# Optimization experiments

Hardware: AMD Instinct MI355X
Metric: run time of the kernel (lower is better)

## Reference

```python
import jax, jax.numpy as jnp
import numpy as np

N = 8192
D = 512            # d_model
E = 8              # num_experts
H = 1024           # expert_hidden_dim
RH = 256           # router_hidden_dim
TOPK = 2
IN_DIM = 9 * D + 3
LN_EPS = 1e-5


def layernorm(x, g, b, eps=LN_EPS):
    m = jnp.mean(x, axis=-1, keepdims=True)
    v = jnp.mean((x - m) ** 2, axis=-1, keepdims=True)
    return (x - m) * jax.lax.rsqrt(v + eps) * g + b


def setup_inputs() -> dict:
    key = jax.random.key(0)
    ks = jax.random.split(key, 16)
    s_in = 1.0 / np.sqrt(IN_DIM)
    s_rh = 1.0 / np.sqrt(RH)
    s_h = 1.0 / np.sqrt(H)
    return {
        "z1": jax.random.normal(ks[0], (N, D), jnp.float32),
        "z2": jax.random.normal(ks[1], (N, D), jnp.float32),
        "z3": jax.random.normal(ks[2], (N, D), jnp.float32),
        "mask": jnp.ones((N, 3), jnp.float32),
        # LayerNorms
        "ln_g": jnp.ones((D,), jnp.float32), "ln_b": jnp.zeros((D,), jnp.float32),
        "lnp_g": jnp.ones((D,), jnp.float32), "lnp_b": jnp.zeros((D,), jnp.float32),
        "oln_g": jnp.ones((D,), jnp.float32), "oln_b": jnp.zeros((D,), jnp.float32),
        # Router MLP
        "r_w1": jax.random.normal(ks[3], (IN_DIM, RH), jnp.float32) * s_in,
        "r_b1": jnp.zeros((RH,), jnp.float32),
        "r_w2": jax.random.normal(ks[4], (RH, E), jnp.float32) * s_rh,
        "r_b2": jnp.zeros((E,), jnp.float32),
        "log_temp": jnp.array(np.log(1.0), jnp.float32),
        # Stacked experts: fc1 [E, IN_DIM, H], fc2 [E, H, D]
        "e_w1": jax.random.normal(ks[5], (E, IN_DIM, H), jnp.float32) * s_in,
        "e_b1": jnp.zeros((E, H), jnp.float32),
        "e_w2": jax.random.normal(ks[6], (E, H, D), jnp.float32) * s_h,
        "e_b2": jnp.zeros((E, D), jnp.float32),
    }


def reference(z1, z2, z3, mask, ln_g, ln_b, lnp_g, lnp_b, oln_g, oln_b,
              r_w1, r_b1, r_w2, r_b2, log_temp, e_w1, e_b1, e_w2, e_b2):
    # --- build fusion input ---
    z1n = layernorm(z1, ln_g, ln_b)
    z2n = layernorm(z2, ln_g, ln_b)
    z3n = layernorm(z3, ln_g, ln_b)
    d12 = layernorm(z1n - z2n, lnp_g, lnp_b)
    d13 = layernorm(z1n - z3n, lnp_g, lnp_b)
    d23 = layernorm(z2n - z3n, lnp_g, lnp_b)
    p12 = layernorm(z1n * z2n, lnp_g, lnp_b)
    p13 = layernorm(z1n * z3n, lnp_g, lnp_b)
    p23 = layernorm(z2n * z3n, lnp_g, lnp_b)
    x = jnp.concatenate([z1n, z2n, z3n, d12, d13, d23, p12, p13, p23, mask], axis=-1)  # [N, 9D+3]

    # --- router: MLP + temperature-scaled top-k softmax ---
    temp = jnp.clip(jnp.exp(log_temp), 1e-3, 100.0)
    rh = jax.nn.gelu(x @ r_w1 + r_b1, approximate=False)
    logits = (rh @ r_w2 + r_b2) / temp                      # [N, E]
    topv, topi = jax.lax.top_k(logits, TOPK)
    keep = jnp.zeros_like(logits).at[jnp.arange(logits.shape[0])[:, None], topi].set(1.0)
    masked_logits = jnp.where(keep == 0, -jnp.inf, logits)
    gate = jax.nn.softmax(masked_logits, axis=-1)           # [N, E]

    # --- dense expert compute (matches torch.stack over experts) ---
    eh = jax.nn.gelu(jnp.einsum('ni,eih->neh', x, e_w1) + e_b1, approximate=False)
    outs = jnp.einsum('neh,ehd->ned', eh, e_w2) + e_b2      # [N, E, D]
    z = jnp.einsum('ne,ned->nd', gate, outs)                # combine

    # --- masked residual ---
    denom = jnp.clip(jnp.sum(mask, axis=1, keepdims=True), 1.0, None)
    z_res = (mask[:, 0:1] * z1n + mask[:, 1:2] * z2n + mask[:, 2:3] * z3n) / denom
    z = z + z_res

    return layernorm(z, oln_g, oln_b)
```

## Files before the change

kernel.cpp:

```cpp
#include <hip/hip_runtime.h>
#include <math.h>

#define N_TOK 8192
#define DMODEL 512
#define NEXP 8
#define HEXP 1024
#define RHDIM 256
#define KP 4672
#define IN_REAL 4611
#define BK 64
#define NPAIR (N_TOK * 2)
#define MAXT 136

typedef unsigned short u16;
typedef __bf16 bf16x8 __attribute__((ext_vector_type(8)));
typedef float f32x4 __attribute__((ext_vector_type(4)));

__device__ inline u16 f2bf(float f) {
    union { float f; unsigned u; } x; x.f = f;
    unsigned r = x.u + 0x7FFFu + ((x.u >> 16) & 1u);
    return (u16)(r >> 16);
}
__device__ inline float bf2f(u16 u) {
    union { unsigned u; float f; } x; x.u = ((unsigned)u) << 16;
    return x.f;
}
__device__ inline float gelu_exact(float v) {
    return 0.5f * v * (1.f + erff(v * 0.70710678118654752440f));
}

__device__ inline void async_cp16(const u16* g, u16* l) {
    __builtin_amdgcn_global_load_lds(
        (const __attribute__((address_space(1))) unsigned int*)g,
        (__attribute__((address_space(3))) unsigned int*)l, 16, 0, 0);
}

template<int M>
__device__ inline void breduce(float (&v)[M], int tid, float* red) {
    #pragma unroll
    for (int o = 32; o > 0; o >>= 1)
        #pragma unroll
        for (int i = 0; i < M; i++) v[i] += __shfl_xor(v[i], o);
    __syncthreads();
    if ((tid & 63) == 0) {
        #pragma unroll
        for (int i = 0; i < M; i++) red[(tid >> 6) * M + i] = v[i];
    }
    __syncthreads();
    if (tid < M) {
        float S = 0.f;
        #pragma unroll
        for (int w8 = 0; w8 < 8; w8++) S += red[w8 * M + tid];
        red[96 + tid] = S;
    }
    __syncthreads();
    #pragma unroll
    for (int i = 0; i < M; i++) v[i] = red[96 + i];
}

__device__ inline float2 bstats512(float v, int tid, float* red) {
    float s = v, q = v * v;
    #pragma unroll
    for (int o = 32; o > 0; o >>= 1) {
        s += __shfl_xor(s, o);
        q += __shfl_xor(q, o);
    }
    __syncthreads();
    if ((tid & 63) == 0) { red[(tid >> 6) * 2] = s; red[(tid >> 6) * 2 + 1] = q; }
    __syncthreads();
    if (tid == 0) {
        float S = 0.f, Q = 0.f;
        #pragma unroll
        for (int i = 0; i < 8; i++) { S += red[i * 2]; Q += red[i * 2 + 1]; }
        float m = S * (1.f / 512.f);
        float var = fmaxf(Q * (1.f / 512.f) - m * m, 0.f);
        red[16] = m;
        red[17] = rsqrtf(var + 1e-5f);
    }
    __syncthreads();
    return make_float2(red[16], red[17]);
}

__global__ __launch_bounds__(256)
void transpose_f32_bf16(const float* __restrict__ src, u16* __restrict__ dhi, u16* __restrict__ dlo,
                        int K0, int KPd, int H, size_t sbatch, size_t dbatch) {
    __shared__ float tile[32][33];
    int bz = blockIdx.z;
    src += (size_t)bz * sbatch;
    size_t dob = (size_t)bz * dbatch;
    int k0 = blockIdx.x * 32, h0 = blockIdx.y * 32;
    int tx = threadIdx.x, ty = threadIdx.y;
    for (int i = ty; i < 32; i += 8) {
        int k = k0 + i;
        tile[i][tx] = (k < K0) ? src[(size_t)k * H + (h0 + tx)] : 0.f;
    }
    __syncthreads();
    for (int i = ty; i < 32; i += 8) {
        int h = h0 + i, k = k0 + tx;
        float v = tile[tx][i];
        u16 hv = f2bf(v);
        dhi[dob + (size_t)h * KPd + k] = hv;
        if (dlo) dlo[dob + (size_t)h * KPd + k] = f2bf(v - bf2f(hv));
    }
}

__global__ __launch_bounds__(512)
void build_x(const float* __restrict__ z1, const float* __restrict__ z2, const float* __restrict__ z3,
             const float* __restrict__ mask,
             const float* __restrict__ ln_g, const float* __restrict__ ln_b,
             const float* __restrict__ lnp_g, const float* __restrict__ lnp_b,
             u16* __restrict__ xhi, u16* __restrict__ xlo) {
    __shared__ float red[108];
    int n = blockIdx.x, d = threadIdx.x;
    float a = z1[(size_t)n * DMODEL + d];
    float b = z2[(size_t)n * DMODEL + d];
    float c = z3[(size_t)n * DMODEL + d];
    float gg = ln_g[d], bb = ln_b[d], pg = lnp_g[d], pb = lnp_b[d];
    size_t base = (size_t)n * KP;

    auto emit = [&](int seg, float v) {
        u16 h = f2bf(v);
        xhi[base + seg * DMODEL + d] = h;
        xlo[base + seg * DMODEL + d] = f2bf(v - bf2f(h));
    };
    auto lnv = [](float v, float s, float q, float g, float bo) {
        float m = s * (1.f / 512.f);
        float var = fmaxf(q * (1.f / 512.f) - m * m, 0.f);
        return (v - m) * rsqrtf(var + 1e-5f) * g + bo;
    };
    float v6[6] = {a, a * a, b, b * b, c, c * c};
    breduce<6>(v6, d, red);
    float z1n = lnv(a, v6[0], v6[1], gg, bb);
    float z2n = lnv(b, v6[2], v6[3], gg, bb);
    float z3n = lnv(c, v6[4], v6[5], gg, bb);
    emit(0, z1n); emit(1, z2n); emit(2, z3n);
    float d12 = z1n - z2n, d13 = z1n - z3n, d23 = z2n - z3n;
    float p12 = z1n * z2n, p13 = z1n * z3n, p23 = z2n * z3n;
    float v12[12] = {d12, d12 * d12, d13, d13 * d13, d23, d23 * d23,
                     p12, p12 * p12, p13, p13 * p13, p23, p23 * p23};
    breduce<12>(v12, d, red);
    emit(3, lnv(d12, v12[0], v12[1], pg, pb));
    emit(4, lnv(d13, v12[2], v12[3], pg, pb));
    emit(5, lnv(d23, v12[4], v12[5], pg, pb));
    emit(6, lnv(p12, v12[6], v12[7], pg, pb));
    emit(7, lnv(p13, v12[8], v12[9], pg, pb));
    emit(8, lnv(p23, v12[10], v12[11], pg, pb));
    if (d < 64) {
        int col = 9 * DMODEL + d;
        float v = (d < 3) ? mask[(size_t)n * 3 + d] : 0.f;
        u16 h = f2bf(v);
        xhi[base + col] = h;
        xlo[base + col] = f2bf(v - bf2f(h));
    }
}


#define GEMM_DEFS                                                             \
    int t = threadIdx.x;                                                      \
    int lane = t & 63, w = t >> 6;                                            \
    int r8 = lane >> 3;                                                       \
    int ce = ((lane & 7) ^ r8) * 8;         \
    int fr = lane & 15, q4 = lane >> 4;                                       \
    int wm = (w & 1) * 64, wn = (w >> 1) * 64;                                \
    f32x4 acc[4][4];                                                          \
    { f32x4 z4 = {0.f, 0.f, 0.f, 0.f};                                        \
      _Pragma("unroll") for (int i = 0; i < 4; i++)                           \
      _Pragma("unroll") for (int j = 0; j < 4; j++) acc[i][j] = z4; }         \
    u16 *lAp[2], *lBp[4];                                                     \
    _Pragma("unroll") for (int i = 0; i < 2; i++)                             \
        lAp[i] = lA + (w * 16 + 8 * i) * BK;                                  \
    _Pragma("unroll") for (int i = 0; i < 4; i++)                             \
        lBp[i] = lB + (w * 32 + 8 * i) * BK;

#define GEMM_KSTEP                                                            \
        __syncthreads();                                                      \
        _Pragma("unroll") for (int i = 0; i < 2; i++) {                       \
            async_cp16(gA[i], lAp[i]); gA[i] += BK;                           \
        }                                                                     \
        _Pragma("unroll") for (int i = 0; i < 4; i++) {                       \
            async_cp16(gB[i], lBp[i]); gB[i] += BK;                           \
        }                                                                     \
        __syncthreads();                                                      \
        _Pragma("unroll") for (int ks = 0; ks < 2; ks++) {                    \
            bf16x8 af[4], bfr[4];                                             \
            int cofs = (((q4 + ks * 4) ^ (fr & 7)) * 8);                      \
            _Pragma("unroll") for (int i = 0; i < 4; i++)                     \
                af[i] = *(const bf16x8*)&lA[(wm + i * 16 + fr) * BK + cofs];  \
            _Pragma("unroll") for (int j = 0; j < 4; j++)                     \
                bfr[j] = *(const bf16x8*)&lB[(wn + j * 16 + fr) * BK + cofs]; \
            _Pragma("unroll") for (int i = 0; i < 4; i++)                     \
            _Pragma("unroll") for (int j = 0; j < 4; j++)                     \
                acc[i][j] = __builtin_amdgcn_mfma_f32_16x16x32_bf16(af[i], bfr[j], acc[i][j], 0, 0, 0); \
        }

__global__ __launch_bounds__(512, 4)
void router_fc1(const u16* __restrict__ xhi, const u16* __restrict__ xlo,
                const u16* __restrict__ rw1hi, const u16* __restrict__ rw1lo,
                float* __restrict__ rpart) {
    int mt = blockIdx.x & 63, part = blockIdx.x >> 6;
    int region = part >> 1, half = part & 1;
    const u16* A = (region == 2) ? xlo : xhi;
    const u16* B = (region == 1) ? rw1lo : rw1hi;
    int kbase = half ? 2304 : 0;
    int klen  = half ? 2368 : 2304;

    __shared__ u16 lA[128 * BK];
    __shared__ u16 lB[256 * BK];
    GEMM_DEFS

    const u16* gA[2]; const u16* gB[4];
    #pragma unroll
    for (int i = 0; i < 2; i++)
        gA[i] = A + (size_t)(mt * 128 + w * 16 + 8 * i + r8) * KP + kbase + ce;
    #pragma unroll
    for (int i = 0; i < 4; i++)
        gB[i] = B + (size_t)(w * 32 + 8 * i + r8) * KP + kbase + ce;

    for (int k0 = 0; k0 < klen; k0 += BK) {
        GEMM_KSTEP
    }
    float* outp = rpart + (size_t)part * ((size_t)N_TOK * RHDIM);
    int cn = lane & 15;
    #pragma unroll
    for (int i = 0; i < 4; i++)
        #pragma unroll
        for (int rr = 0; rr < 4; rr++) {
            int mg = mt * 128 + wm + i * 16 + q4 * 4 + rr;
            #pragma unroll
            for (int j = 0; j < 4; j++)
                outp[(size_t)mg * RHDIM + wn + j * 16 + cn] = acc[i][j][rr];
        }
}

__global__ __launch_bounds__(256)
void logits_topk(const float* __restrict__ rpart, const float* __restrict__ r_b1,
                 const float* __restrict__ r_w2, const float* __restrict__ r_b2,
                 const float* __restrict__ log_temp,
                 float* __restrict__ pgate, int* __restrict__ pexp,
                 int* __restrict__ lists, int* __restrict__ counts) {
    int t = threadIdx.x, wave = t >> 6, lane = t & 63;
    int n = blockIdx.x * 4 + wave;
    float4 v = {0.f, 0.f, 0.f, 0.f};
    #pragma unroll
    for (int p = 0; p < 6; p++) {
        float4 s = ((const float4*)(rpart + (size_t)p * ((size_t)N_TOK * RHDIM) + (size_t)n * RHDIM))[lane];
        v.x += s.x; v.y += s.y; v.z += s.z; v.w += s.w;
    }
    float4 b1 = ((const float4*)r_b1)[lane];
    float rh0 = gelu_exact(v.x + b1.x);
    float rh1 = gelu_exact(v.y + b1.y);
    float rh2 = gelu_exact(v.z + b1.z);
    float rh3 = gelu_exact(v.w + b1.w);
    int k = lane * 4;
    float p8[8];
    #pragma unroll
    for (int e = 0; e < 8; e++)
        p8[e] = rh0 * r_w2[(k + 0) * 8 + e] + rh1 * r_w2[(k + 1) * 8 + e]
              + rh2 * r_w2[(k + 2) * 8 + e] + rh3 * r_w2[(k + 3) * 8 + e];
    #pragma unroll
    for (int o = 32; o > 0; o >>= 1)
        #pragma unroll
        for (int e = 0; e < 8; e++) p8[e] += __shfl_xor(p8[e], o);
    if (lane == 0) {
        float temp = fminf(fmaxf(expf(log_temp[0]), 1e-3f), 100.f);
        float l[8];
        #pragma unroll
        for (int e = 0; e < 8; e++) l[e] = (p8[e] + r_b2[e]) / temp;
        int i1 = 0;
        #pragma unroll
        for (int i = 1; i < 8; i++) if (l[i] > l[i1]) i1 = i;
        int i2 = (i1 == 0) ? 1 : 0;
        #pragma unroll
        for (int i = 0; i < 8; i++) if (i != i1 && l[i] > l[i2]) i2 = i;
        float p = expf(l[i2] - l[i1]);
        float g1 = 1.f / (1.f + p);
        float g2 = p / (1.f + p);
        pgate[n * 2] = g1;     pexp[n * 2] = i1;
        pgate[n * 2 + 1] = g2; pexp[n * 2 + 1] = i2;
        int pos1 = atomicAdd(&counts[i1], 1);
        lists[(size_t)i1 * N_TOK + pos1] = n * 2;
        int pos2 = atomicAdd(&counts[i2], 1);
        lists[(size_t)i2 * N_TOK + pos2] = n * 2 + 1;
    }
}

__global__ void sched_tiles(const int* __restrict__ counts, int* __restrict__ tiles) {
    if (threadIdx.x == 0) {
        int tcount = 0;
        for (int e = 0; e < NEXP; e++) {
            int nt = (counts[e] + 127) >> 7;
            for (int mt = 0; mt < nt; mt++) tiles[tcount++] = (e << 16) | mt;
        }
        for (; tcount < MAXT; tcount++) tiles[tcount] = -1;
    }
}

__global__ __launch_bounds__(512, 4)
void expert_fc1(const u16* __restrict__ xhi, const u16* __restrict__ w1t,
                const float* __restrict__ e_b1, const int* __restrict__ lists,
                const int* __restrict__ counts, const int* __restrict__ tiles,
                u16* __restrict__ eh) {
    int nt = blockIdx.x & 3, ti = blockIdx.x >> 2;
    int info = tiles[ti];
    if (info < 0) return;
    int e = info >> 16, mt = info & 0xFFFF;
    int cnt = counts[e];

    __shared__ u16 lA[128 * BK];
    __shared__ u16 lB[256 * BK];
    __shared__ int rows[128];
    int tt = threadIdx.x;
    if (tt < 128) {
        int m = mt * 128 + tt;
        rows[tt] = lists[(size_t)e * N_TOK + (m < cnt ? m : 0)];
    }
    __syncthreads();

    GEMM_DEFS

    const u16* wb = w1t + (size_t)e * HEXP * KP + (size_t)(nt * 256) * KP;
    const u16* gA[2]; const u16* gB[4];
    #pragma unroll
    for (int i = 0; i < 2; i++)
        gA[i] = xhi + (size_t)(rows[w * 16 + 8 * i + r8] >> 1) * KP + ce;
    #pragma unroll
    for (int i = 0; i < 4; i++)
        gB[i] = wb + (size_t)(w * 32 + 8 * i + r8) * KP + ce;

    for (int k0 = 0; k0 < KP; k0 += BK) {
        GEMM_KSTEP
    }
    int cn = lane & 15;
    #pragma unroll
    for (int i = 0; i < 4; i++)
        #pragma unroll
        for (int rr = 0; rr < 4; rr++) {
            int ml = wm + i * 16 + q4 * 4 + rr;
            int mg = mt * 128 + ml;
            if (mg < cnt) {
                int entry = rows[ml];
                #pragma unroll
                for (int j = 0; j < 4; j++) {
                    int col = nt * 256 + wn + j * 16 + cn;
                    float v = acc[i][j][rr] + e_b1[(size_t)e * HEXP + col];
                    eh[(size_t)entry * HEXP + col] = f2bf(gelu_exact(v));
                }
            }
        }
}

__global__ __launch_bounds__(512, 4)
void expert_fc2(const u16* __restrict__ eh, const u16* __restrict__ w2t,
                const int* __restrict__ lists, const int* __restrict__ counts,
                const int* __restrict__ tiles, float* __restrict__ outs) {
    int nt = blockIdx.x & 1, ti = blockIdx.x >> 1;
    int info = tiles[ti];
    if (info < 0) return;
    int e = info >> 16, mt = info & 0xFFFF;
    int cnt = counts[e];

    __shared__ u16 lA[128 * BK];
    __shared__ u16 lB[256 * BK];
    __shared__ int rows[128];
    int tt = threadIdx.x;
    if (tt < 128) {
        int m = mt * 128 + tt;
        rows[tt] = lists[(size_t)e * N_TOK + (m < cnt ? m : 0)];
    }
    __syncthreads();

    GEMM_DEFS

    const u16* wb = w2t + (size_t)e * DMODEL * HEXP + (size_t)(nt * 256) * HEXP;
    const u16* gA[2]; const u16* gB[4];
    #pragma unroll
    for (int i = 0; i < 2; i++)
        gA[i] = eh + (size_t)rows[w * 16 + 8 * i + r8] * HEXP + ce;
    #pragma unroll
    for (int i = 0; i < 4; i++)
        gB[i] = wb + (size_t)(w * 32 + 8 * i + r8) * HEXP + ce;

    for (int k0 = 0; k0 < HEXP; k0 += BK) {
        GEMM_KSTEP
    }
    int cn = lane & 15;
    #pragma unroll
    for (int i = 0; i < 4; i++)
        #pragma unroll
        for (int rr = 0; rr < 4; rr++) {
            int ml = wm + i * 16 + q4 * 4 + rr;
            int mg = mt * 128 + ml;
            if (mg < cnt) {
                int entry = rows[ml];
                #pragma unroll
                for (int j = 0; j < 4; j++) {
                    int col = nt * 256 + wn + j * 16 + cn;
                    outs[(size_t)entry * DMODEL + col] = acc[i][j][rr];
                }
            }
        }
}

__global__ __launch_bounds__(512)
void combine_ln(const float* __restrict__ outs, const float* __restrict__ pgate,
                const int* __restrict__ pexp, const float* __restrict__ e_b2,
                const float* __restrict__ mask, const u16* __restrict__ xhi,
                const u16* __restrict__ xlo, const float* __restrict__ oln_g,
                const float* __restrict__ oln_b, float* __restrict__ out) {
    __shared__ float red[18];
    int n = blockIdx.x, d = threadIdx.x;
    float g0 = pgate[n * 2], g1 = pgate[n * 2 + 1];
    int e0 = pexp[n * 2], e1 = pexp[n * 2 + 1];
    float o = g0 * (outs[(size_t)(n * 2) * DMODEL + d] + e_b2[(size_t)e0 * DMODEL + d])
            + g1 * (outs[(size_t)(n * 2 + 1) * DMODEL + d] + e_b2[(size_t)e1 * DMODEL + d]);
    float m0 = mask[n * 3 + 0], m1 = mask[n * 3 + 1], m2 = mask[n * 3 + 2];
    float denom = fmaxf(m0 + m1 + m2, 1.f);
    size_t xb = (size_t)n * KP;
    float z1n = bf2f(xhi[xb + d]) + bf2f(xlo[xb + d]);
    float z2n = bf2f(xhi[xb + DMODEL + d]) + bf2f(xlo[xb + DMODEL + d]);
    float z3n = bf2f(xhi[xb + 2 * DMODEL + d]) + bf2f(xlo[xb + 2 * DMODEL + d]);
    float z = o + (m0 * z1n + m1 * z2n + m2 * z3n) / denom;
    float2 st = bstats512(z, d, red);
    out[(size_t)n * DMODEL + d] = (z - st.x) * st.y * oln_g[d] + oln_b[d];
}

extern "C" void kernel_launch(void* const* d_in, const int* in_sizes, int n_in,
                              void* d_out, int out_size, void* d_ws, size_t ws_size,
                              hipStream_t stream) {
    (void)in_sizes; (void)n_in; (void)out_size; (void)ws_size;
    const float* z1       = (const float*)d_in[0];
    const float* z2       = (const float*)d_in[1];
    const float* z3       = (const float*)d_in[2];
    const float* mask     = (const float*)d_in[3];
    const float* ln_g     = (const float*)d_in[4];
    const float* ln_b     = (const float*)d_in[5];
    const float* lnp_g    = (const float*)d_in[6];
    const float* lnp_b    = (const float*)d_in[7];
    const float* oln_g    = (const float*)d_in[8];
    const float* oln_b    = (const float*)d_in[9];
    const float* r_w1     = (const float*)d_in[10];
    const float* r_b1     = (const float*)d_in[11];
    const float* r_w2     = (const float*)d_in[12];
    const float* r_b2     = (const float*)d_in[13];
    const float* log_temp = (const float*)d_in[14];
    const float* e_w1     = (const float*)d_in[15];
    const float* e_b1     = (const float*)d_in[16];
    const float* e_w2     = (const float*)d_in[17];
    const float* e_b2     = (const float*)d_in[18];
    float* out = (float*)d_out;

    char* p = (char*)d_ws;
    auto carve = [&](size_t bytes) { char* r = p; p += (bytes + 255) & ~(size_t)255; return r; };
    u16*   xhi    = (u16*)carve((size_t)N_TOK * KP * 2);
    u16*   xlo    = (u16*)carve((size_t)N_TOK * KP * 2);
    u16*   w1t    = (u16*)carve((size_t)NEXP * HEXP * KP * 2);
    u16*   w2t    = (u16*)carve((size_t)NEXP * DMODEL * HEXP * 2);
    u16*   rw1hi  = (u16*)carve((size_t)RHDIM * KP * 2);
    u16*   rw1lo  = (u16*)carve((size_t)RHDIM * KP * 2);
    float* rpart  = (float*)carve((size_t)6 * N_TOK * RHDIM * 4);
    u16*   eh     = (u16*)carve((size_t)NPAIR * HEXP * 2);
    float* outsb  = (float*)carve((size_t)NPAIR * DMODEL * 4);
    float* pgate  = (float*)carve((size_t)NPAIR * 4);
    int*   pexp   = (int*)carve((size_t)NPAIR * 4);
    int*   lists  = (int*)carve((size_t)NEXP * N_TOK * 4);
    int*   counts = (int*)carve(256);
    int*   tiles  = (int*)carve(MAXT * 4);

    dim3 tb(32, 8);
    transpose_f32_bf16<<<dim3(KP / 32, HEXP / 32, NEXP), tb, 0, stream>>>(
        e_w1, w1t, (u16*)nullptr, IN_REAL, KP, HEXP, (size_t)IN_REAL * HEXP, (size_t)HEXP * KP);
    transpose_f32_bf16<<<dim3(HEXP / 32, DMODEL / 32, NEXP), tb, 0, stream>>>(
        e_w2, w2t, (u16*)nullptr, HEXP, HEXP, DMODEL, (size_t)HEXP * DMODEL, (size_t)DMODEL * HEXP);
    transpose_f32_bf16<<<dim3(KP / 32, RHDIM / 32, 1), tb, 0, stream>>>(
        r_w1, rw1hi, rw1lo, IN_REAL, KP, RHDIM, (size_t)0, (size_t)0);

    build_x<<<N_TOK, 512, 0, stream>>>(z1, z2, z3, mask, ln_g, ln_b, lnp_g, lnp_b, xhi, xlo);

    router_fc1<<<384, 512, 0, stream>>>(xhi, xlo, rw1hi, rw1lo, rpart);

    hipMemsetAsync(counts, 0, 256, stream);
    logits_topk<<<N_TOK / 4, 256, 0, stream>>>(rpart, r_b1, r_w2, r_b2, log_temp,
                                               pgate, pexp, lists, counts);
    sched_tiles<<<1, 64, 0, stream>>>(counts, tiles);

    expert_fc1<<<MAXT * 4, 512, 0, stream>>>(xhi, w1t, e_b1, lists, counts, tiles, eh);
    expert_fc2<<<MAXT * 2, 512, 0, stream>>>(eh, w2t, lists, counts, tiles, outsb);

    combine_ln<<<N_TOK, 512, 0, stream>>>(outsb, pgate, pexp, e_b2, mask, xhi, xlo, oln_g, oln_b, out);
}
```

Measured before the change: 991.5 us.

## Triple-buffer LDS tiles with async prefetch in router and expert GEMMs

Replaces the single-buffered load-sync-compute loop in the router fc1 and both expert GEMMs with a 3-stage LDS ring. Async global-to-LDS copies are issued three K-steps ahead, and vmcnt waits let loads overlap the MFMA work. Fragments are read into registers before the next stage is issued, and the MFMA block runs at raised wave priority. LDS use triples (about 144KB per block), so launch bounds drop from 4 to 2 blocks per CU. This trades occupancy for latency hiding, and the clamped tail prefetch repeats redundant loads.

```diff
diff --git a/kernel.cpp b/kernel.cpp
--- a/kernel.cpp
+++ b/kernel.cpp
@@ -155,9 +155,12 @@
 }
 
 
-#define GEMM_DEFS                                                             \
-    int t = threadIdx.x;                                                      \
-    int lane = t & 63, w = t >> 6;                                            \
+#define ASZ (128 * BK)
+#define BSZ (256 * BK)
+
+#define PIPE_DEFS                                                             \
+    int t_ = threadIdx.x;                                                     \
+    int lane = t_ & 63, w = t_ >> 6;                                          \
     int r8 = lane >> 3;                                                       \
     int ce = ((lane & 7) ^ r8) * 8;         \
     int fr = lane & 15, q4 = lane >> 4;                                       \
@@ -166,34 +169,54 @@
     { f32x4 z4 = {0.f, 0.f, 0.f, 0.f};                                        \
       _Pragma("unroll") for (int i = 0; i < 4; i++)                           \
       _Pragma("unroll") for (int j = 0; j < 4; j++) acc[i][j] = z4; }         \
-    u16 *lAp[2], *lBp[4];                                                     \
+    u16 *lApA[2], *lApB[4];                                                   \
     _Pragma("unroll") for (int i = 0; i < 2; i++)                             \
-        lAp[i] = lA + (w * 16 + 8 * i) * BK;                                  \
+        lApA[i] = lA + (w * 16 + 8 * i) * BK;                                 \
     _Pragma("unroll") for (int i = 0; i < 4; i++)                             \
-        lBp[i] = lB + (w * 32 + 8 * i) * BK;
-
-#define GEMM_KSTEP                                                            \
-        __syncthreads();                                                      \
-        _Pragma("unroll") for (int i = 0; i < 2; i++) {                       \
-            async_cp16(gA[i], lAp[i]); gA[i] += BK;                           \
-        }                                                                     \
-        _Pragma("unroll") for (int i = 0; i < 4; i++) {                       \
-            async_cp16(gB[i], lBp[i]); gB[i] += BK;                           \
-        }                                                                     \
-        __syncthreads();                                                      \
+        lApB[i] = lB + (w * 32 + 8 * i) * BK;
+
+#define PIPE_STAGE(buf_, kk_)                                                 \
+    { int ko_ = (kk_) * BK;                                                   \
+      _Pragma("unroll") for (int i = 0; i < 2; i++)                           \
+          async_cp16(gA[i] + ko_, lApA[i] + (buf_) * ASZ);                    \
+      _Pragma("unroll") for (int i = 0; i < 4; i++)                           \
+          async_cp16(gB[i] + ko_, lApB[i] + (buf_) * BSZ); }
+
+#define PIPE_LOOP(NT_)                                                        \
+    PIPE_STAGE(0, 0)                                                          \
+    PIPE_STAGE(1, 1)                                                          \
+    PIPE_STAGE(2, 2)                                                          \
+    int cur = 0;                                                              \
+    for (int kt = 0; kt < (NT_); kt++) {                                      \
+        asm volatile("s_waitcnt vmcnt(12)" ::: "memory");                     \
+        __builtin_amdgcn_sched_barrier(0);                                    \
+        __builtin_amdgcn_s_barrier();                                         \
+        const u16* cA = lA + cur * ASZ;                                       \
+        const u16* cB = lB + cur * BSZ;                                       \
+        bf16x8 af[2][4], bfr[2][4];                                           \
         _Pragma("unroll") for (int ks = 0; ks < 2; ks++) {                    \
-            bf16x8 af[4], bfr[4];                                             \
             int cofs = (((q4 + ks * 4) ^ (fr & 7)) * 8);                      \
             _Pragma("unroll") for (int i = 0; i < 4; i++)                     \
-                af[i] = *(const bf16x8*)&lA[(wm + i * 16 + fr) * BK + cofs];  \
+                af[ks][i] = *(const bf16x8*)&cA[(wm + i * 16 + fr) * BK + cofs]; \
             _Pragma("unroll") for (int j = 0; j < 4; j++)                     \
-                bfr[j] = *(const bf16x8*)&lB[(wn + j * 16 + fr) * BK + cofs]; \
-            _Pragma("unroll") for (int i = 0; i < 4; i++)                     \
-            _Pragma("unroll") for (int j = 0; j < 4; j++)                     \
-                acc[i][j] = __builtin_amdgcn_mfma_f32_16x16x32_bf16(af[i], bfr[j], acc[i][j], 0, 0, 0); \
-        }
-
-__global__ __launch_bounds__(512, 4)
+                bfr[ks][j] = *(const bf16x8*)&cB[(wn + j * 16 + fr) * BK + cofs]; \
+        }                                                                     \
+        asm volatile("s_waitcnt lgkmcnt(0)" ::: "memory");                    \
+        __builtin_amdgcn_sched_barrier(0);                                    \
+        __builtin_amdgcn_s_barrier();                                         \
+        int nk = kt + 3; if (nk >= (NT_)) nk = (NT_) - 1;                     \
+        PIPE_STAGE(cur, nk)                                                   \
+        __builtin_amdgcn_sched_barrier(0);                                    \
+        __builtin_amdgcn_s_setprio(1);                                        \
+        _Pragma("unroll") for (int ks = 0; ks < 2; ks++)                      \
+        _Pragma("unroll") for (int i = 0; i < 4; i++)                         \
+        _Pragma("unroll") for (int j = 0; j < 4; j++)                         \
+            acc[i][j] = __builtin_amdgcn_mfma_f32_16x16x32_bf16(af[ks][i], bfr[ks][j], acc[i][j], 0, 0, 0); \
+        __builtin_amdgcn_s_setprio(0);                                        \
+        cur = (cur == 2) ? 0 : cur + 1;                                       \
+    }
+
+__global__ __launch_bounds__(512, 2)
 void router_fc1(const u16* __restrict__ xhi, const u16* __restrict__ xlo,
                 const u16* __restrict__ rw1hi, const u16* __restrict__ rw1lo,
                 float* __restrict__ rpart) {
@@ -204,9 +227,9 @@
     int kbase = half ? 2304 : 0;
     int klen  = half ? 2368 : 2304;
 
-    __shared__ u16 lA[128 * BK];
-    __shared__ u16 lB[256 * BK];
-    GEMM_DEFS
+    __shared__ u16 lA[3 * ASZ];
+    __shared__ u16 lB[3 * BSZ];
+    PIPE_DEFS
 
     const u16* gA[2]; const u16* gB[4];
     #pragma unroll
@@ -216,9 +239,9 @@
     for (int i = 0; i < 4; i++)
         gB[i] = B + (size_t)(w * 32 + 8 * i + r8) * KP + kbase + ce;
 
-    for (int k0 = 0; k0 < klen; k0 += BK) {
-        GEMM_KSTEP
-    }
+    int nt = klen / BK;
+    PIPE_LOOP(nt)
+
     float* outp = rpart + (size_t)part * ((size_t)N_TOK * RHDIM);
     int cn = lane & 15;
     #pragma unroll
@@ -295,7 +318,7 @@
     }
 }
 
-__global__ __launch_bounds__(512, 4)
+__global__ __launch_bounds__(512, 2)
 void expert_fc1(const u16* __restrict__ xhi, const u16* __restrict__ w1t,
                 const float* __restrict__ e_b1, const int* __restrict__ lists,
                 const int* __restrict__ counts, const int* __restrict__ tiles,
@@ -306,8 +329,8 @@
     int e = info >> 16, mt = info & 0xFFFF;
     int cnt = counts[e];
 
-    __shared__ u16 lA[128 * BK];
-    __shared__ u16 lB[256 * BK];
+    __shared__ u16 lA[3 * ASZ];
+    __shared__ u16 lB[3 * BSZ];
     __shared__ int rows[128];
     int tt = threadIdx.x;
     if (tt < 128) {
@@ -316,7 +339,7 @@
     }
     __syncthreads();
 
-    GEMM_DEFS
+    PIPE_DEFS
 
     const u16* wb = w1t + (size_t)e * HEXP * KP + (size_t)(nt * 256) * KP;
     const u16* gA[2]; const u16* gB[4];
@@ -327,9 +350,8 @@
     for (int i = 0; i < 4; i++)
         gB[i] = wb + (size_t)(w * 32 + 8 * i + r8) * KP + ce;
 
-    for (int k0 = 0; k0 < KP; k0 += BK) {
-        GEMM_KSTEP
-    }
+    PIPE_LOOP(KP / BK)
+
     int cn = lane & 15;
     #pragma unroll
     for (int i = 0; i < 4; i++)
@@ -349,7 +371,7 @@
         }
 }
 
-__global__ __launch_bounds__(512, 4)
+__global__ __launch_bounds__(512, 2)
 void expert_fc2(const u16* __restrict__ eh, const u16* __restrict__ w2t,
                 const int* __restrict__ lists, const int* __restrict__ counts,
                 const int* __restrict__ tiles, float* __restrict__ outs) {
@@ -359,8 +381,8 @@
     int e = info >> 16, mt = info & 0xFFFF;
     int cnt = counts[e];
 
-    __shared__ u16 lA[128 * BK];
-    __shared__ u16 lB[256 * BK];
+    __shared__ u16 lA[3 * ASZ];
+    __shared__ u16 lB[3 * BSZ];
     __shared__ int rows[128];
     int tt = threadIdx.x;
     if (tt < 128) {
@@ -369,7 +391,7 @@
     }
     __syncthreads();
 
-    GEMM_DEFS
+    PIPE_DEFS
 
     const u16* wb = w2t + (size_t)e * DMODEL * HEXP + (size_t)(nt * 256) * HEXP;
     const u16* gA[2]; const u16* gB[4];
@@ -380,9 +402,8 @@
     for (int i = 0; i < 4; i++)
         gB[i] = wb + (size_t)(w * 32 + 8 * i + r8) * HEXP + ce;
 
-    for (int k0 = 0; k0 < HEXP; k0 += BK) {
-        GEMM_KSTEP
-    }
+    PIPE_LOOP(HEXP / BK)
+
     int cn = lane & 15;
     #pragma unroll
     for (int i = 0; i < 4; i++)
```

Result: slower. 1.051 ms (+6.0%).

## Use 256x256 double-buffered tiles in expert fc1 with separate tile schedule

Applied to the files above, without the earlier changes.

Expert fc1 now processes 256-row M tiles instead of 128, with each warp computing 128x64 outputs (8x4 MFMA accumulators). It double-buffers A and B tiles in shared memory using async copies and a vmcnt wait, so the next K tile loads while the current one is computed. A second tile list built with 256-row granularity drives the launch, and the bias is hoisted into registers. The intent is to reuse each weight tile across more rows and hide global load latency; the cost is more register and LDS pressure (occupancy bound lowered to 2) and more padding waste per expert.

```diff
diff --git a/kernel.cpp b/kernel.cpp
--- a/kernel.cpp
+++ b/kernel.cpp
@@ -11,6 +11,7 @@
 #define BK 64
 #define NPAIR (N_TOK * 2)
 #define MAXT 136
+#define MAXT2 72
 
 typedef unsigned short u16;
 typedef __bf16 bf16x8 __attribute__((ext_vector_type(8)));
@@ -154,7 +155,6 @@
     }
 }
 
-
 #define GEMM_DEFS                                                             \
     int t = threadIdx.x;                                                      \
     int lane = t & 63, w = t >> 6;                                            \
@@ -284,7 +284,8 @@
     }
 }
 
-__global__ void sched_tiles(const int* __restrict__ counts, int* __restrict__ tiles) {
+__global__ void sched_tiles(const int* __restrict__ counts, int* __restrict__ tiles,
+                            int* __restrict__ tiles2) {
     if (threadIdx.x == 0) {
         int tcount = 0;
         for (int e = 0; e < NEXP; e++) {
@@ -293,56 +294,132 @@
         }
         for (; tcount < MAXT; tcount++) tiles[tcount] = -1;
     }
-}
-
-__global__ __launch_bounds__(512, 4)
+    if (threadIdx.x == 1) {
+        int tcount = 0;
+        for (int e = 0; e < NEXP; e++) {
+            int nt = (counts[e] + 255) >> 8;
+            for (int mt = 0; mt < nt; mt++) tiles2[tcount++] = (e << 16) | mt;
+        }
+        for (; tcount < MAXT2; tcount++) tiles2[tcount] = -1;
+    }
+}
+
+#define TSZ (256 * BK)
+
+__global__ __launch_bounds__(512, 2)
 void expert_fc1(const u16* __restrict__ xhi, const u16* __restrict__ w1t,
                 const float* __restrict__ e_b1, const int* __restrict__ lists,
-                const int* __restrict__ counts, const int* __restrict__ tiles,
+                const int* __restrict__ counts, const int* __restrict__ tiles2,
                 u16* __restrict__ eh) {
     int nt = blockIdx.x & 3, ti = blockIdx.x >> 2;
-    int info = tiles[ti];
+    int info = tiles2[ti];
     if (info < 0) return;
     int e = info >> 16, mt = info & 0xFFFF;
     int cnt = counts[e];
 
-    __shared__ u16 lA[128 * BK];
-    __shared__ u16 lB[256 * BK];
-    __shared__ int rows[128];
+    __shared__ u16 lA[2 * TSZ];
+    __shared__ u16 lB[2 * TSZ];
+    __shared__ int rows[256];
     int tt = threadIdx.x;
-    if (tt < 128) {
-        int m = mt * 128 + tt;
+    if (tt < 256) {
+        int m = mt * 256 + tt;
         rows[tt] = lists[(size_t)e * N_TOK + (m < cnt ? m : 0)];
     }
     __syncthreads();
 
-    GEMM_DEFS
-
+    int lane = tt & 63, w = tt >> 6;
+    int r8 = lane >> 3;
+    int ce = ((lane & 7) ^ r8) * 8;
+    int fr = lane & 15, q4 = lane >> 4;
+    int wm = (w & 1) * 128, wn = (w >> 1) * 64;
+
+    f32x4 acc[8][4];
+    { f32x4 z4 = {0.f, 0.f, 0.f, 0.f};
+      #pragma unroll
+      for (int i = 0; i < 8; i++)
+          #pragma unroll
+          for (int j = 0; j < 4; j++) acc[i][j] = z4; }
+
+    u16 *sA[4], *sB[4];
+    #pragma unroll
+    for (int i = 0; i < 4; i++) {
+        sA[i] = lA + (w * 32 + 8 * i) * BK;
+        sB[i] = lB + (w * 32 + 8 * i) * BK;
+    }
     const u16* wb = w1t + (size_t)e * HEXP * KP + (size_t)(nt * 256) * KP;
-    const u16* gA[2]; const u16* gB[4];
-    #pragma unroll
-    for (int i = 0; i < 2; i++)
-        gA[i] = xhi + (size_t)(rows[w * 16 + 8 * i + r8] >> 1) * KP + ce;
-    #pragma unroll
-    for (int i = 0; i < 4; i++)
+    const u16* gA[4]; const u16* gB[4];
+    #pragma unroll
+    for (int i = 0; i < 4; i++) {
+        gA[i] = xhi + (size_t)(rows[w * 32 + 8 * i + r8] >> 1) * KP + ce;
         gB[i] = wb + (size_t)(w * 32 + 8 * i + r8) * KP + ce;
-
-    for (int k0 = 0; k0 < KP; k0 += BK) {
-        GEMM_KSTEP
-    }
+    }
+
+    #pragma unroll
+    for (int i = 0; i < 4; i++) {
+        async_cp16(gA[i], sA[i]); async_cp16(gB[i], sB[i]);
+        gA[i] += BK; gB[i] += BK;
+    }
+
+    const int NT = KP / BK;
+    int cur = 0;
+    for (int kt = 0; kt < NT; kt++) {
+        int nb = cur ^ 1;
+        if (kt + 1 < NT) {
+            #pragma unroll
+            for (int i = 0; i < 4; i++) {
+                async_cp16(gA[i], sA[i] + nb * TSZ); async_cp16(gB[i], sB[i] + nb * TSZ);
+                gA[i] += BK; gB[i] += BK;
+            }
+        } else {
+            #pragma unroll
+            for (int i = 0; i < 4; i++) {
+                async_cp16(gA[i] - BK, sA[i] + nb * TSZ); async_cp16(gB[i] - BK, sB[i] + nb * TSZ);
+            }
+        }
+        asm volatile("s_waitcnt vmcnt(8)" ::: "memory");
+        __builtin_amdgcn_s_barrier();
+        __builtin_amdgcn_sched_barrier(0);
+        const u16* cA = lA + cur * TSZ;
+        const u16* cB = lB + cur * TSZ;
+        #pragma unroll
+        for (int ks = 0; ks < 2; ks++) {
+            bf16x8 af[8]; bf16x8 bfr[4];
+            int cofs = ((q4 + ks * 4) ^ (fr & 7)) * 8;
+            #pragma unroll
+            for (int j = 0; j < 4; j++)
+                bfr[j] = *(const bf16x8*)&cB[(wn + j * 16 + fr) * BK + cofs];
+            #pragma unroll
+            for (int i = 0; i < 8; i++)
+                af[i] = *(const bf16x8*)&cA[(wm + i * 16 + fr) * BK + cofs];
+            __builtin_amdgcn_s_setprio(1);
+            #pragma unroll
+            for (int i = 0; i < 8; i++)
+                #pragma unroll
+                for (int j = 0; j < 4; j++)
+                    acc[i][j] = __builtin_amdgcn_mfma_f32_16x16x32_bf16(af[i], bfr[j], acc[i][j], 0, 0, 0);
+            __builtin_amdgcn_s_setprio(0);
+        }
+        __builtin_amdgcn_s_barrier();
+        cur = nb;
+    }
+
     int cn = lane & 15;
-    #pragma unroll
-    for (int i = 0; i < 4; i++)
+    float b1v[4];
+    #pragma unroll
+    for (int j = 0; j < 4; j++)
+        b1v[j] = e_b1[(size_t)e * HEXP + nt * 256 + wn + j * 16 + cn];
+    #pragma unroll
+    for (int i = 0; i < 8; i++)
         #pragma unroll
         for (int rr = 0; rr < 4; rr++) {
             int ml = wm + i * 16 + q4 * 4 + rr;
-            int mg = mt * 128 + ml;
+            int mg = mt * 256 + ml;
             if (mg < cnt) {
                 int entry = rows[ml];
                 #pragma unroll
                 for (int j = 0; j < 4; j++) {
                     int col = nt * 256 + wn + j * 16 + cn;
-                    float v = acc[i][j][rr] + e_b1[(size_t)e * HEXP + col];
+                    float v = acc[i][j][rr] + b1v[j];
                     eh[(size_t)entry * HEXP + col] = f2bf(gelu_exact(v));
                 }
             }
@@ -465,6 +542,7 @@
     int*   lists  = (int*)carve((size_t)NEXP * N_TOK * 4);
     int*   counts = (int*)carve(256);
     int*   tiles  = (int*)carve(MAXT * 4);
+    int*   tiles2 = (int*)carve(MAXT2 * 4);
 
     dim3 tb(32, 8);
     transpose_f32_bf16<<<dim3(KP / 32, HEXP / 32, NEXP), tb, 0, stream>>>(
@@ -481,9 +559,9 @@
     hipMemsetAsync(counts, 0, 256, stream);
     logits_topk<<<N_TOK / 4, 256, 0, stream>>>(rpart, r_b1, r_w2, r_b2, log_temp,
                                                pgate, pexp, lists, counts);
-    sched_tiles<<<1, 64, 0, stream>>>(counts, tiles);
-
-    expert_fc1<<<MAXT * 4, 512, 0, stream>>>(xhi, w1t, e_b1, lists, counts, tiles, eh);
+    sched_tiles<<<1, 64, 0, stream>>>(counts, tiles, tiles2);
+
+    expert_fc1<<<MAXT2 * 4, 512, 0, stream>>>(xhi, w1t, e_b1, lists, counts, tiles2, eh);
     expert_fc2<<<MAXT * 2, 512, 0, stream>>>(eh, w2t, lists, counts, tiles, outsb);
 
     combine_ln<<<N_TOK, 512, 0, stream>>>(outsb, pgate, pexp, e_b2, mask, xhi, xlo, oln_g, oln_b, out);
```

New measurement: 1.072 ms. 1.08x slower.
